# Optimization experiments

Measured on AMD Instinct MI355X. Metric: run time of the kernel, lower is better.

## Reference

```python
import jax, jax.numpy as jnp
import numpy as np
import math

HEADS = 4
LN_EPS = 1e-5


def _layer_norm(x, gamma, beta):
    # LayerNorm over last dim (N=4096), matching nn.LayerNorm(4096)
    mu = jnp.mean(x, axis=-1, keepdims=True)
    var = jnp.mean((x - mu) ** 2, axis=-1, keepdims=True)
    return (x - mu) * jax.lax.rsqrt(var + LN_EPS) * gamma + beta


def setup_inputs() -> dict:
    key = jax.random.key(0)
    ks = jax.random.split(key, 10)
    L, IMG, N = 1024, 1024, 4096
    s_img = 1.0 / math.sqrt(IMG)
    s_L = 1.0 / math.sqrt(L)
    return {
        "point_features": jax.random.normal(ks[0], (1, L, N), jnp.float32),
        "img_features": jax.random.normal(ks[1], (1, IMG, N), jnp.float32),
        # 4 per-head 1x1 convs IMG_chl -> L_chl
        "W_img": jax.random.normal(ks[2], (HEADS, L, IMG), jnp.float32) * s_img,
        "b_img": jax.random.normal(ks[3], (HEADS, L), jnp.float32) * s_img,
        # conv_L: L_chl -> L_chl
        "W_L": jax.random.normal(ks[4], (L, L), jnp.float32) * s_L,
        "b_L": jax.random.normal(ks[5], (L,), jnp.float32) * s_L,
        # LayerNorm(4096)
        "ln_g": jnp.ones((N,), jnp.float32),
        "ln_b": jnp.zeros((N,), jnp.float32),
        # conv_fusion: L_chl -> L_chl
        "W_f": jax.random.normal(ks[6], (L, L), jnp.float32) * s_L,
        "b_f": jax.random.normal(ks[7], (L,), jnp.float32) * s_L,
    }


def reference(point_features, img_features, W_img, b_img, W_L, b_L, ln_g, ln_b, W_f, b_f):
    # L_query = conv_L(point_features): [1, L, N]
    L_query = jnp.einsum('oi,bin->bon', W_L, point_features) + b_L[None, :, None]
    dk = L_query.shape[1]
    N = L_query.shape[2]

    # All 4 head keys at once: [H, 1, L, N]
    keys = jnp.einsum('hoi,bin->hbon', W_img, img_features) + b_img[:, None, :, None]

    # score_i = sum_c(key_i * query) / sqrt(dk)  -> cat over heads: [H, N] (B=1)
    score = jnp.sum(keys * L_query[None], axis=2).reshape(HEADS, N) / jnp.sqrt(jnp.float32(dk))

    # softmax across heads (dim=0), weightmap = [1, H, N]
    weight = jax.nn.softmax(score, axis=0)
    weightmap = weight[None]

    # z = sum_h weight[h] * key_h : [1, L, N]
    z = jnp.einsum('hn,hbcn->bcn', weight, keys)

    fused = _layer_norm(z + L_query, ln_g, ln_b)
    fusion_features = jnp.einsum('oi,bin->bon', W_f, fused) + b_f[None, :, None]
    return (fusion_features, weightmap)
```

## Files before the change

### kernel.cpp

```cpp
#include <hip/hip_runtime.h>
#include <hip/hip_bf16.h>
#include <stdint.h>

using u16 = unsigned short;

typedef __attribute__((ext_vector_type(8))) short bf16x8;
typedef __attribute__((ext_vector_type(4))) float f32x4;

typedef const __attribute__((address_space(1))) unsigned int* gas_t;
typedef __attribute__((address_space(3))) unsigned int* las_t;

__device__ inline void g2l16(const u16* g, u16* l) {
  __builtin_amdgcn_global_load_lds((gas_t)g, (las_t)l, 16, 0, 0);
}

__device__ inline u16 f2b(float x) {
  union { float f; uint32_t u; } v; v.f = x;
  uint32_t r = (v.u + 0x7FFFu + ((v.u >> 16) & 1u)) >> 16;
  return (u16)r;
}
__device__ inline float b2f(u16 b) {
  union { uint32_t u; float f; } v; v.u = ((uint32_t)b) << 16;
  return v.f;
}
__device__ inline float b2f_lo(uint32_t p) {
  union { uint32_t u; float f; } v; v.u = p << 16; return v.f;
}
__device__ inline float b2f_hi(uint32_t p) {
  union { uint32_t u; float f; } v; v.u = p & 0xFFFF0000u; return v.f;
}

__device__ inline void store_out(float* p, float v) { *p = v; }
__device__ inline void store_out(u16* p, float v) { *p = f2b(v); }

template<typename OutT>
__device__ inline void gemm_tile_128(const u16* __restrict__ A,
                                     const u16* __restrict__ Bt,
                                     const float* __restrict__ bias,
                                     OutT* __restrict__ C,
                                     int m0, int n0, int N, int K,
                                     u16* As, u16* Bs)
{
  const int tid  = threadIdx.x;
  const int wave = tid >> 6;
  const int lane = tid & 63;
  const int wm = wave >> 1, wn = wave & 1;
  const int lr = lane & 15;
  const int lq = lane >> 4;
  const int x7 = lr & 7;

  const int srow = tid >> 3;
  const int sgc  = (tid & 7) ^ (srow & 7);
  const u16* gA = A  + (size_t)(m0 + srow) * K + sgc * 8;
  const u16* gB = Bt + (size_t)(n0 + srow) * K + sgc * 8;
  u16* dstA = As + wave * 512;
  u16* dstB = Bs + wave * 512;

  f32x4 acc[4][4];
  #pragma unroll
  for (int i = 0; i < 4; ++i)
    #pragma unroll
    for (int j = 0; j < 4; ++j)
      acc[i][j] = (f32x4){0.f, 0.f, 0.f, 0.f};

  for (int k0 = 0; k0 < K; k0 += 64) {
    #pragma unroll
    for (int s = 0; s < 4; ++s) {
      g2l16(gA + (size_t)(s * 32) * K + k0, dstA + s * 2048);
      g2l16(gB + (size_t)(s * 32) * K + k0, dstB + s * 2048);
    }
    __syncthreads();

    #pragma unroll
    for (int ks = 0; ks < 2; ++ks) {
      const int pa = (ks * 4 + lq) ^ x7;
      bf16x8 af[4], bfr[4];
      #pragma unroll
      for (int im = 0; im < 4; ++im)
        af[im] = *(const bf16x8*)&As[(wm * 64 + im * 16 + lr) * 64 + pa * 8];
      #pragma unroll
      for (int in = 0; in < 4; ++in)
        bfr[in] = *(const bf16x8*)&Bs[(wn * 64 + in * 16 + lr) * 64 + pa * 8];

      #pragma unroll
      for (int im = 0; im < 4; ++im)
        #pragma unroll
        for (int in = 0; in < 4; ++in)
          acc[im][in] = __builtin_amdgcn_mfma_f32_16x16x32_bf16(
              af[im], bfr[in], acc[im][in], 0, 0, 0);
    }
    __syncthreads();
  }

  #pragma unroll
  for (int im = 0; im < 4; ++im) {
    const int mbase = m0 + wm * 64 + im * 16 + lq * 4;
    #pragma unroll
    for (int in = 0; in < 4; ++in) {
      const int ncol = n0 + wn * 64 + in * 16 + lr;
      #pragma unroll
      for (int r = 0; r < 4; ++r) {
        const int m = mbase + r;
        store_out(C + (size_t)m * N + ncol, acc[im][in][r] + bias[m]);
      }
    }
  }
}

__global__ __launch_bounds__(256)
void gemm_keys_q(const u16* __restrict__ WIb, const u16* __restrict__ IT,
                 const float* __restrict__ bim, u16* __restrict__ KEYS,
                 const u16* __restrict__ WLb, const u16* __restrict__ PT,
                 const float* __restrict__ bL, u16* __restrict__ Qb)
{
  __shared__ u16 As[128 * 64];
  __shared__ u16 Bs[128 * 64];
  const int by = blockIdx.y;
  const bool keys = (by < 32);
  const u16*   A    = keys ? WIb : WLb;
  const u16*   Bt   = keys ? IT  : PT;
  const float* bias = keys ? bim : bL;
  u16*         C    = keys ? KEYS : Qb;
  const int m0 = (by & 31) * 128;
  const int n0 = blockIdx.x * 128;
  gemm_tile_128<u16>(A, Bt, bias, C, m0, n0, 4096, 1024, As, Bs);
}

template<typename OutT>
__global__ __launch_bounds__(256)
void gemm_bt_64(const u16* __restrict__ A, const u16* __restrict__ Bt,
                const float* __restrict__ bias, OutT* __restrict__ C,
                int M, int N, int K)
{
  __shared__ u16 As[64 * 64];
  __shared__ u16 Bs[128 * 64];

  const int tid  = threadIdx.x;
  const int wave = tid >> 6;
  const int lane = tid & 63;
  const int lr = lane & 15;
  const int lq = lane >> 4;
  const int x7 = lr & 7;

  const int m0 = blockIdx.y * 64;
  const int n0 = blockIdx.x * 128;

  const int srow = tid >> 3;
  const int sgc  = (tid & 7) ^ (srow & 7);
  const u16* gA = A  + (size_t)(m0 + srow) * K + sgc * 8;
  const u16* gB = Bt + (size_t)(n0 + srow) * K + sgc * 8;
  u16* dstA = As + wave * 512;
  u16* dstB = Bs + wave * 512;

  f32x4 acc[4][2];
  #pragma unroll
  for (int i = 0; i < 4; ++i)
    #pragma unroll
    for (int j = 0; j < 2; ++j)
      acc[i][j] = (f32x4){0.f, 0.f, 0.f, 0.f};

  for (int k0 = 0; k0 < K; k0 += 64) {
    #pragma unroll
    for (int s = 0; s < 2; ++s)
      g2l16(gA + (size_t)(s * 32) * K + k0, dstA + s * 2048);
    #pragma unroll
    for (int s = 0; s < 4; ++s)
      g2l16(gB + (size_t)(s * 32) * K + k0, dstB + s * 2048);
    __syncthreads();

    #pragma unroll
    for (int ks = 0; ks < 2; ++ks) {
      const int pa = (ks * 4 + lq) ^ x7;
      bf16x8 af[4], bfr[2];
      #pragma unroll
      for (int im = 0; im < 4; ++im)
        af[im] = *(const bf16x8*)&As[(im * 16 + lr) * 64 + pa * 8];
      #pragma unroll
      for (int in = 0; in < 2; ++in)
        bfr[in] = *(const bf16x8*)&Bs[(wave * 32 + in * 16 + lr) * 64 + pa * 8];

      #pragma unroll
      for (int im = 0; im < 4; ++im)
        #pragma unroll
        for (int in = 0; in < 2; ++in)
          acc[im][in] = __builtin_amdgcn_mfma_f32_16x16x32_bf16(
              af[im], bfr[in], acc[im][in], 0, 0, 0);
    }
    __syncthreads();
  }

  #pragma unroll
  for (int im = 0; im < 4; ++im) {
    const int mbase = m0 + im * 16 + lq * 4;
    #pragma unroll
    for (int in = 0; in < 2; ++in) {
      const int ncol = n0 + wave * 32 + in * 16 + lr;
      #pragma unroll
      for (int r = 0; r < 4; ++r) {
        const int m = mbase + r;
        store_out(C + (size_t)m * N + ncol, acc[im][in][r] + bias[m]);
      }
    }
  }
}

__global__ __launch_bounds__(256)
void prep(const float* __restrict__ P, u16* __restrict__ PT,
          const float* __restrict__ I, u16* __restrict__ IT,
          const float4* __restrict__ wim, const float4* __restrict__ wl,
          const float4* __restrict__ wf, ushort4* __restrict__ wimb,
          ushort4* __restrict__ wlb, ushort4* __restrict__ wfb)
{
  const int bid = blockIdx.x;
  if (bid < 2048) {
    const int z   = bid >> 10;
    const int rem = bid & 1023;
    const int ct  = rem & 63;
    const int rt  = rem >> 6;
    const float* in = z ? I : P;
    u16* out = z ? IT : PT;
    __shared__ u16 tile[64][72];
    const int r0 = rt * 64, c0 = ct * 64;
    const int tr  = threadIdx.x >> 4;
    const int tc4 = threadIdx.x & 15;
    #pragma unroll
    for (int it = 0; it < 4; ++it) {
      const int r = it * 16 + tr;
      const float4 v = *(const float4*)&in[(size_t)(r0 + r) * 4096 + c0 + tc4 * 4];
      ushort4 o;
      o.x = f2b(v.x); o.y = f2b(v.y); o.z = f2b(v.z); o.w = f2b(v.w);
      *(ushort4*)&tile[r][tc4 * 4] = o;
    }
    __syncthreads();
    #pragma unroll
    for (int it = 0; it < 4; ++it) {
      const int c = it * 16 + tr;
      ushort4 o;
      o.x = tile[tc4 * 4 + 0][c];
      o.y = tile[tc4 * 4 + 1][c];
      o.z = tile[tc4 * 4 + 2][c];
      o.w = tile[tc4 * 4 + 3][c];
      *(ushort4*)&out[(size_t)(c0 + c) * 1024 + r0 + tc4 * 4] = o;
    }
  } else {
    int i = (bid - 2048) * 256 + threadIdx.x;
    const float4* src; ushort4* dst;
    if (i < 1048576)      { src = wim; dst = wimb; }
    else if (i < 1310720) { src = wl;  dst = wlb;  i -= 1048576; }
    else                  { src = wf;  dst = wfb;  i -= 1310720; }
    const float4 v = src[i];
    ushort4 o;
    o.x = f2b(v.x); o.y = f2b(v.y); o.z = f2b(v.z); o.w = f2b(v.w);
    dst[i] = o;
  }
}

__global__ __launch_bounds__(256)
void transpose_u16(const u16* __restrict__ in, u16* __restrict__ out,
                   int R, int C)
{
  __shared__ u16 tile[64][72];
  const int c0 = blockIdx.x * 64, r0 = blockIdx.y * 64;
  const int tr  = threadIdx.x >> 4;
  const int tc4 = threadIdx.x & 15;
  #pragma unroll
  for (int it = 0; it < 4; ++it) {
    const int r = it * 16 + tr;
    *(ushort4*)&tile[r][tc4 * 4] =
        *(const ushort4*)&in[(size_t)(r0 + r) * C + c0 + tc4 * 4];
  }
  __syncthreads();
  #pragma unroll
  for (int it = 0; it < 4; ++it) {
    const int c = it * 16 + tr;
    ushort4 o;
    o.x = tile[tc4 * 4 + 0][c];
    o.y = tile[tc4 * 4 + 1][c];
    o.z = tile[tc4 * 4 + 2][c];
    o.w = tile[tc4 * 4 + 3][c];
    *(ushort4*)&out[(size_t)(c0 + c) * R + r0 + tc4 * 4] = o;
  }
}

__global__ __launch_bounds__(256)
void score_partial(const u16* __restrict__ keys, const u16* __restrict__ Qb,
                   float* __restrict__ part)
{
  const int n  = blockIdx.x * 1024 + threadIdx.x * 4;
  const int c0 = blockIdx.y * 16;
  float s[4][4];
  #pragma unroll
  for (int h = 0; h < 4; ++h)
    #pragma unroll
    for (int e = 0; e < 4; ++e) s[h][e] = 0.f;

  for (int c = c0; c < c0 + 16; ++c) {
    const uint2 qv = *(const uint2*)&Qb[(size_t)c * 4096 + n];
    const float q0 = b2f_lo(qv.x), q1 = b2f_hi(qv.x);
    const float q2 = b2f_lo(qv.y), q3 = b2f_hi(qv.y);
    #pragma unroll
    for (int h = 0; h < 4; ++h) {
      const uint2 kv = *(const uint2*)&keys[((size_t)((h << 10) + c)) * 4096 + n];
      s[h][0] = fmaf(q0, b2f_lo(kv.x), s[h][0]);
      s[h][1] = fmaf(q1, b2f_hi(kv.x), s[h][1]);
      s[h][2] = fmaf(q2, b2f_lo(kv.y), s[h][2]);
      s[h][3] = fmaf(q3, b2f_hi(kv.y), s[h][3]);
    }
  }
  #pragma unroll
  for (int h = 0; h < 4; ++h) {
    float4 o;
    o.x = s[h][0] * 0.03125f; o.y = s[h][1] * 0.03125f;
    o.z = s[h][2] * 0.03125f; o.w = s[h][3] * 0.03125f;
    *(float4*)&part[((size_t)(blockIdx.y * 4 + h)) * 4096 + n] = o;
  }
}

__global__ __launch_bounds__(256)
void softmax_h(const float* __restrict__ part, float* __restrict__ wmap)
{
  const int n = blockIdx.x * 256 + threadIdx.x;
  float s0 = 0.f, s1 = 0.f, s2 = 0.f, s3 = 0.f;
  #pragma unroll 4
  for (int cy = 0; cy < 64; ++cy) {
    const float* p = part + (size_t)cy * 16384 + n;
    s0 += p[0]; s1 += p[4096]; s2 += p[8192]; s3 += p[12288];
  }
  const float m = fmaxf(fmaxf(s0, s1), fmaxf(s2, s3));
  const float e0 = expf(s0 - m), e1 = expf(s1 - m);
  const float e2 = expf(s2 - m), e3 = expf(s3 - m);
  const float inv = 1.f / (e0 + e1 + e2 + e3);
  wmap[n] = e0 * inv; wmap[4096 + n] = e1 * inv;
  wmap[8192 + n] = e2 * inv; wmap[12288 + n] = e3 * inv;
}

__global__ __launch_bounds__(256)
void z_ln(const u16* __restrict__ keys, const u16* __restrict__ Qb,
          const float* __restrict__ w, const float* __restrict__ g,
          const float* __restrict__ bb, u16* __restrict__ fused)
{
  const int c  = blockIdx.x;
  const int tx = threadIdx.x;
  float t[16];
  float s = 0.f, s2 = 0.f;
  #pragma unroll
  for (int j = 0; j < 2; ++j) {
    const int n = tx * 8 + j * 2048;
    const uint4 qv = *(const uint4*)&Qb[(size_t)c * 4096 + n];
    float z[8] = {0.f,0.f,0.f,0.f,0.f,0.f,0.f,0.f};
    #pragma unroll
    for (int h = 0; h < 4; ++h) {
      const uint4 kv = *(const uint4*)&keys[((size_t)((h << 10) + c)) * 4096 + n];
      const float4 w0 = *(const float4*)&w[h * 4096 + n];
      const float4 w1 = *(const float4*)&w[h * 4096 + n + 4];
      z[0] = fmaf(w0.x, b2f_lo(kv.x), z[0]);
      z[1] = fmaf(w0.y, b2f_hi(kv.x), z[1]);
      z[2] = fmaf(w0.z, b2f_lo(kv.y), z[2]);
      z[3] = fmaf(w0.w, b2f_hi(kv.y), z[3]);
      z[4] = fmaf(w1.x, b2f_lo(kv.z), z[4]);
      z[5] = fmaf(w1.y, b2f_hi(kv.z), z[5]);
      z[6] = fmaf(w1.z, b2f_lo(kv.w), z[6]);
      z[7] = fmaf(w1.w, b2f_hi(kv.w), z[7]);
    }
    const uint32_t qs[4] = {qv.x, qv.y, qv.z, qv.w};
    #pragma unroll
    for (int e = 0; e < 4; ++e) {
      const float v0 = z[2 * e]     + b2f_lo(qs[e]);
      const float v1 = z[2 * e + 1] + b2f_hi(qs[e]);
      t[8 * j + 2 * e]     = v0;
      t[8 * j + 2 * e + 1] = v1;
      s += v0 + v1;
      s2 = fmaf(v0, v0, fmaf(v1, v1, s2));
    }
  }
  #pragma unroll
  for (int o = 32; o > 0; o >>= 1) {
    s  += __shfl_down(s, o);
    s2 += __shfl_down(s2, o);
  }
  __shared__ float rbuf[8];
  const int wave = tx >> 6, lane = tx & 63;
  if (lane == 0) { rbuf[wave] = s; rbuf[4 + wave] = s2; }
  __syncthreads();
  s  = rbuf[0] + rbuf[1] + rbuf[2] + rbuf[3];
  s2 = rbuf[4] + rbuf[5] + rbuf[6] + rbuf[7];
  const float mu  = s * (1.f / 4096.f);
  const float var = s2 * (1.f / 4096.f) - mu * mu;
  const float rs  = rsqrtf(var + 1e-5f);
  #pragma unroll
  for (int j = 0; j < 2; ++j) {
    const int n = tx * 8 + j * 2048;
    #pragma unroll
    for (int q4 = 0; q4 < 2; ++q4) {
      const float4 gv = *(const float4*)&g[n + 4 * q4];
      const float4 bv = *(const float4*)&bb[n + 4 * q4];
      ushort4 o;
      o.x = f2b((t[8 * j + 4 * q4]     - mu) * rs * gv.x + bv.x);
      o.y = f2b((t[8 * j + 4 * q4 + 1] - mu) * rs * gv.y + bv.y);
      o.z = f2b((t[8 * j + 4 * q4 + 2] - mu) * rs * gv.z + bv.z);
      o.w = f2b((t[8 * j + 4 * q4 + 3] - mu) * rs * gv.w + bv.w);
      *(ushort4*)&fused[(size_t)c * 4096 + n + 4 * q4] = o;
    }
  }
}

extern "C" void kernel_launch(void* const* d_in, const int* in_sizes, int n_in,
                              void* d_out, int out_size, void* d_ws, size_t ws_size,
                              hipStream_t stream)
{
  const float* P   = (const float*)d_in[0];
  const float* I   = (const float*)d_in[1];
  const float* Wim = (const float*)d_in[2];
  const float* bim = (const float*)d_in[3];
  const float* WL  = (const float*)d_in[4];
  const float* bL  = (const float*)d_in[5];
  const float* lng = (const float*)d_in[6];
  const float* lnb = (const float*)d_in[7];
  const float* Wf  = (const float*)d_in[8];
  const float* bf_ = (const float*)d_in[9];
  float* out = (float*)d_out;

  char* ws = (char*)d_ws;
  u16*   PT     = (u16*)(ws + 0);
  u16*   IT     = (u16*)(ws + (size_t)8  * 1048576);
  u16*   WLb    = (u16*)(ws + (size_t)16 * 1048576);
  u16*   WIb    = (u16*)(ws + (size_t)18 * 1048576);
  u16*   WFb    = (u16*)(ws + (size_t)26 * 1048576);
  u16*   Qb     = (u16*)(ws + (size_t)28 * 1048576);
  u16*   KEYS   = (u16*)(ws + (size_t)36 * 1048576);
  float* PART   = (float*)(ws + 0);
  u16*   FUSED  = (u16*)(ws + (size_t)70 * 1048576);
  u16*   FUSEDT = (u16*)(ws + (size_t)78 * 1048576);

  const dim3 b256(256);

  prep<<<8192, b256, 0, stream>>>(P, PT, I, IT,
                                  (const float4*)Wim, (const float4*)WL,
                                  (const float4*)Wf, (ushort4*)WIb,
                                  (ushort4*)WLb, (ushort4*)WFb);

  gemm_keys_q<<<dim3(32, 40), b256, 0, stream>>>(WIb, IT, bim, KEYS,
                                                 WLb, PT, bL, Qb);

  score_partial<<<dim3(4, 64), b256, 0, stream>>>(KEYS, Qb, PART);
  float* wmap = out + (size_t)1024 * 4096;
  softmax_h<<<16, b256, 0, stream>>>(PART, wmap);

  z_ln<<<1024, b256, 0, stream>>>(KEYS, Qb, wmap, lng, lnb, FUSED);
  transpose_u16<<<dim3(64, 16), b256, 0, stream>>>(FUSED, FUSEDT, 1024, 4096);

  gemm_bt_64<float><<<dim3(32, 16), b256, 0, stream>>>(WFb, FUSEDT, bf_, out, 1024, 4096, 1024);
}
```

Baseline: 217.8 us.

## Rewrite keys/query GEMM as 256x256 double-buffered 8-wave pipelined kernel

Replaces the 128x128 single-buffered GEMM for keys and query with a 256x256 tile per 512-thread block. The LDS is double-buffered so the next K slice is prefetched with global_load_lds while the current slice feeds MFMAs, and the inner loop is split into four phases separated by barriers, with s_setprio raised around the MFMA bursts. The goal is to hide global load latency behind compute and to reuse more data per tile. In exchange it needs 128KB of LDS and many accumulator registers per block, and launches only 320 blocks, which may limit occupancy and leave some CUs with uneven work.

```diff
diff --git a/kernel.cpp b/kernel.cpp
--- a/kernel.cpp
+++ b/kernel.cpp
@@ -33,18 +33,35 @@
 __device__ inline void store_out(float* p, float v) { *p = v; }
 __device__ inline void store_out(u16* p, float v) { *p = f2b(v); }
 
-template<typename OutT>
-__device__ inline void gemm_tile_128(const u16* __restrict__ A,
-                                     const u16* __restrict__ Bt,
-                                     const float* __restrict__ bias,
-                                     OutT* __restrict__ C,
-                                     int m0, int n0, int N, int K,
-                                     u16* As, u16* Bs)
-{
+#define CFENCE asm volatile("" ::: "memory")
+
+__global__ __launch_bounds__(512)
+void gemm_keys_q(const u16* __restrict__ WIb, const u16* __restrict__ IT,
+                 const float* __restrict__ bim, u16* __restrict__ KEYS,
+                 const u16* __restrict__ WLb, const u16* __restrict__ PT,
+                 const float* __restrict__ bL, u16* __restrict__ Qb)
+{
+  __shared__ u16 As[2][256 * 64];
+  __shared__ u16 Bs[2][256 * 64];
+
+  const int K  = 1024;
+  const int NT = 16;
+  const int N  = 4096;
+
+  const int by = blockIdx.y;
+  const bool keys = (by < 16);
+  const u16*   A    = keys ? WIb : WLb;
+  const u16*   Bt   = keys ? IT  : PT;
+  const float* bias = keys ? bim : bL;
+  u16*         C    = keys ? KEYS : Qb;
+  const int m0 = (keys ? by : (by - 16)) * 256;
+  const int n0 = blockIdx.x * 256;
+
   const int tid  = threadIdx.x;
   const int wave = tid >> 6;
   const int lane = tid & 63;
-  const int wm = wave >> 1, wn = wave & 1;
+  const int wm = wave >> 2;
+  const int wn = wave & 3;
   const int lr = lane & 15;
   const int lq = lane >> 4;
   const int x7 = lr & 7;
@@ -53,77 +70,91 @@
   const int sgc  = (tid & 7) ^ (srow & 7);
   const u16* gA = A  + (size_t)(m0 + srow) * K + sgc * 8;
   const u16* gB = Bt + (size_t)(n0 + srow) * K + sgc * 8;
-  u16* dstA = As + wave * 512;
-  u16* dstB = Bs + wave * 512;
-
-  f32x4 acc[4][4];
-  #pragma unroll
-  for (int i = 0; i < 4; ++i)
+  const int ldst = wave * 512;
+
+  f32x4 acc[8][4];
+  #pragma unroll
+  for (int i = 0; i < 8; ++i)
     #pragma unroll
     for (int j = 0; j < 4; ++j)
       acc[i][j] = (f32x4){0.f, 0.f, 0.f, 0.f};
 
-  for (int k0 = 0; k0 < K; k0 += 64) {
-    #pragma unroll
-    for (int s = 0; s < 4; ++s) {
-      g2l16(gA + (size_t)(s * 32) * K + k0, dstA + s * 2048);
-      g2l16(gB + (size_t)(s * 32) * K + k0, dstB + s * 2048);
-    }
-    __syncthreads();
-
-    #pragma unroll
-    for (int ks = 0; ks < 2; ++ks) {
-      const int pa = (ks * 4 + lq) ^ x7;
-      bf16x8 af[4], bfr[4];
-      #pragma unroll
-      for (int im = 0; im < 4; ++im)
-        af[im] = *(const bf16x8*)&As[(wm * 64 + im * 16 + lr) * 64 + pa * 8];
-      #pragma unroll
-      for (int in = 0; in < 4; ++in)
-        bfr[in] = *(const bf16x8*)&Bs[(wn * 64 + in * 16 + lr) * 64 + pa * 8];
-
-      #pragma unroll
-      for (int im = 0; im < 4; ++im)
+  #pragma unroll
+  for (int r = 0; r < 4; ++r) {
+    g2l16(gA + (size_t)(r * 64) * K, &As[0][r * 4096 + ldst]);
+    g2l16(gB + (size_t)(r * 64) * K, &Bs[0][r * 4096 + ldst]);
+  }
+  asm volatile("s_waitcnt vmcnt(0)" ::: "memory");
+  __builtin_amdgcn_s_barrier();
+  CFENCE;
+
+  bf16x8 bfr[4];
+
+  #pragma unroll 2
+  for (int t = 0; t < NT; ++t) {
+    const int cur = t & 1;
+    const u16* Ab = As[cur];
+    const u16* Bb = Bs[cur];
+    u16* An = (u16*)As[cur ^ 1];
+    u16* Bn = (u16*)Bs[cur ^ 1];
+    const size_t knext = (size_t)(t + 1) * 64;
+    const bool more = (t + 1 < NT);
+
+    #pragma unroll
+    for (int p = 0; p < 4; ++p) {
+      const int ksp = p >> 1;
+      const int imh = p & 1;
+      if (more) {
+        if (p < 2) {
+          g2l16(gA + (size_t)((2 * p)     * 64) * K + knext, &An[(2 * p)     * 4096 + ldst]);
+          g2l16(gA + (size_t)((2 * p + 1) * 64) * K + knext, &An[(2 * p + 1) * 4096 + ldst]);
+        } else {
+          g2l16(gB + (size_t)((2 * p - 4) * 64) * K + knext, &Bn[(2 * p - 4) * 4096 + ldst]);
+          g2l16(gB + (size_t)((2 * p - 3) * 64) * K + knext, &Bn[(2 * p - 3) * 4096 + ldst]);
+        }
+      }
+      const int pa = ((ksp * 4 + lq) ^ x7) * 8;
+      bf16x8 af[4];
+      #pragma unroll
+      for (int i = 0; i < 4; ++i)
+        af[i] = *(const bf16x8*)&Ab[(wm * 128 + imh * 64 + i * 16 + lr) * 64 + pa];
+      if (imh == 0) {
         #pragma unroll
-        for (int in = 0; in < 4; ++in)
-          acc[im][in] = __builtin_amdgcn_mfma_f32_16x16x32_bf16(
-              af[im], bfr[in], acc[im][in], 0, 0, 0);
-    }
-    __syncthreads();
-  }
-
-  #pragma unroll
-  for (int im = 0; im < 4; ++im) {
-    const int mbase = m0 + wm * 64 + im * 16 + lq * 4;
-    #pragma unroll
-    for (int in = 0; in < 4; ++in) {
-      const int ncol = n0 + wn * 64 + in * 16 + lr;
+        for (int j = 0; j < 4; ++j)
+          bfr[j] = *(const bf16x8*)&Bb[(wn * 64 + j * 16 + lr) * 64 + pa];
+      }
+      CFENCE;
+      __builtin_amdgcn_s_barrier();
+      CFENCE;
+      __builtin_amdgcn_s_setprio(1);
+      #pragma unroll
+      for (int i = 0; i < 4; ++i)
+        #pragma unroll
+        for (int j = 0; j < 4; ++j)
+          acc[imh * 4 + i][j] = __builtin_amdgcn_mfma_f32_16x16x32_bf16(
+              af[i], bfr[j], acc[imh * 4 + i][j], 0, 0, 0);
+      __builtin_amdgcn_s_setprio(0);
+      if (p == 3)
+        asm volatile("s_waitcnt vmcnt(0)" ::: "memory");
+      CFENCE;
+      __builtin_amdgcn_s_barrier();
+      CFENCE;
+    }
+  }
+
+  #pragma unroll
+  for (int mf = 0; mf < 8; ++mf) {
+    const int mbase = m0 + wm * 128 + (mf >> 2) * 64 + (mf & 3) * 16 + lq * 4;
+    #pragma unroll
+    for (int j = 0; j < 4; ++j) {
+      const int ncol = n0 + wn * 64 + j * 16 + lr;
       #pragma unroll
       for (int r = 0; r < 4; ++r) {
         const int m = mbase + r;
-        store_out(C + (size_t)m * N + ncol, acc[im][in][r] + bias[m]);
+        store_out(C + (size_t)m * N + ncol, acc[mf][j][r] + bias[m]);
       }
     }
   }
-}
-
-__global__ __launch_bounds__(256)
-void gemm_keys_q(const u16* __restrict__ WIb, const u16* __restrict__ IT,
-                 const float* __restrict__ bim, u16* __restrict__ KEYS,
-                 const u16* __restrict__ WLb, const u16* __restrict__ PT,
-                 const float* __restrict__ bL, u16* __restrict__ Qb)
-{
-  __shared__ u16 As[128 * 64];
-  __shared__ u16 Bs[128 * 64];
-  const int by = blockIdx.y;
-  const bool keys = (by < 32);
-  const u16*   A    = keys ? WIb : WLb;
-  const u16*   Bt   = keys ? IT  : PT;
-  const float* bias = keys ? bim : bL;
-  u16*         C    = keys ? KEYS : Qb;
-  const int m0 = (by & 31) * 128;
-  const int n0 = blockIdx.x * 128;
-  gemm_tile_128<u16>(A, Bt, bias, C, m0, n0, 4096, 1024, As, Bs);
 }
 
 template<typename OutT>
@@ -439,8 +470,8 @@
                                   (const float4*)Wf, (ushort4*)WIb,
                                   (ushort4*)WLb, (ushort4*)WFb);
 
-  gemm_keys_q<<<dim3(32, 40), b256, 0, stream>>>(WIb, IT, bim, KEYS,
-                                                 WLb, PT, bL, Qb);
+  gemm_keys_q<<<dim3(16, 20), dim3(512), 0, stream>>>(WIb, IT, bim, KEYS,
+                                                      WLb, PT, bL, Qb);
 
   score_partial<<<dim3(4, 64), b256, 0, stream>>>(KEYS, Qb, PART);
   float* wmap = out + (size_t)1024 * 4096;
```

Result: slower. 241.9 us (+11.1%).
